# Performance work log

Hardware: AMD Instinct MI355X
Metric: run time of the kernel (lower is better)

The kernel has to match this reference:

```python
import jax, jax.numpy as jnp
import numpy as np

B, S, D, H = 4, 2048, 1024, 16
DQ = D // H  # 64


def setup_inputs() -> dict:
    key = jax.random.key(0)
    ks = jax.random.split(key, 7)
    return {
        "q": jax.random.normal(ks[0], (B, S, D), dtype=jnp.float32),
        "k": jax.random.normal(ks[1], (B, S, D), dtype=jnp.float32),
        "v": jax.random.normal(ks[2], (B, S, D), dtype=jnp.float32),
        "mask": jax.random.randint(ks[3], (B, 1, S, S), 0, 2, dtype=jnp.int32),
        "weight_q": jax.random.normal(ks[4], (H, D, DQ), dtype=jnp.float32),
        "weight_k": jax.random.normal(ks[5], (H, D, DQ), dtype=jnp.float32),
        "weight_v": jax.random.normal(ks[6], (H, D, DQ), dtype=jnp.float32),
    }


def reference(q, k, v, mask, weight_q, weight_k, weight_v):
    # Per-head projections: [b,s,d] x [h,d,q] -> [b,h,s,q]
    Q = jnp.einsum('bsd,hdq->bhsq', q, weight_q)
    K = jnp.einsum('bsd,hdq->bhsq', k, weight_k)
    V = jnp.einsum('bsd,hdq->bhsq', v, weight_v)
    scale = 1.0 / jnp.sqrt(jnp.float32(DQ))
    scores = jnp.einsum('bhsq,bhtq->bhst', Q, K) * scale  # [b,h,s,s]
    scores = jnp.where(mask == 0, jnp.float32(-1e9), scores)
    scores = jax.nn.softmax(scores, axis=-1)
    # Faithful to torch.einsum('bhss,bhsq->bhsq', ...): repeated index 's'
    # takes the DIAGONAL of the attention matrix, scaling V elementwise.
    diag = jnp.diagonal(scores, axis1=2, axis2=3)  # [b,h,s]
    x = diag[..., None] * V  # [b,h,s,dq]
    return x
```

## Files before the change

kernel.cpp:

```cpp
#include <hip/hip_runtime.h>


#define BB 4
#define SS 2048
#define DD 1024
#define HH 16
#define DQQ 64

typedef unsigned short u16;
typedef unsigned int u32;
typedef __attribute__((ext_vector_type(8))) short bf16x8;
typedef __attribute__((ext_vector_type(4))) float f32x4;

static constexpr float SCALE_L2E = 0.125f * 1.44269504f;
static constexpr float NEG9 = -1e9f;

#define MFMA16(a, b, c) __builtin_amdgcn_mfma_f32_16x16x32_bf16((a), (b), (c), 0, 0, 0)

__device__ __forceinline__ float ex2(float x) {
#if __has_builtin(__builtin_amdgcn_exp2f)
    return __builtin_amdgcn_exp2f(x);
#else
    return __expf(x * 0.69314718055994531f);
#endif
}

__device__ __forceinline__ u16 bfrne(float x) {
    u32 u = __float_as_uint(x);
    return (u16)((u + 0x7fffu + ((u >> 16) & 1u)) >> 16);
}
__device__ __forceinline__ u32 pk2(float a, float b) {
    return (u32)bfrne(a) | ((u32)bfrne(b) << 16);
}
__device__ __forceinline__ float lo_f(u32 p) { return __uint_as_float(p << 16); }
__device__ __forceinline__ float hi_f(u32 p) { return __uint_as_float(p & 0xFFFF0000u); }

union U4V { u32 u[4]; bf16x8 v; uint4 q4; };

__global__ __launch_bounds__(256) void mask_pack_k(const int* __restrict__ mask,
                                                   u32* __restrict__ bits) {
    const int w = blockIdx.x * 256 + threadIdx.x;
    const long long row  = (long long)(w >> 6);
    const long long base = row * SS + (long long)((w & 63) << 5);
    const int4* mp = reinterpret_cast<const int4*>(mask + base);
    u32 v = 0;
#pragma unroll
    for (int j = 0; j < 8; ++j) {
        int4 m4 = mp[j];
        v |= (m4.x != 0 ? 1u : 0u) << (4 * j + 0);
        v |= (m4.y != 0 ? 1u : 0u) << (4 * j + 1);
        v |= (m4.z != 0 ? 1u : 0u) << (4 * j + 2);
        v |= (m4.w != 0 ? 1u : 0u) << (4 * j + 3);
    }
    bits[w] = v;
}

__global__ __launch_bounds__(256) void wsplit2_k(const float* __restrict__ W,
                                                 u16* __restrict__ Ph,
                                                 u16* __restrict__ Pl,
                                                 int has_lo, float scale) {
    const int f = blockIdx.x * 4 + (threadIdx.x >> 6);
    const int lane = threadIdx.x & 63;
    const int qtile = f >> 5, kc = f & 31;
    const int h = qtile >> 2, q = ((qtile & 3) << 4) + (lane & 15);
    const int d0 = kc * 32 + (lane >> 4) * 8;
    float x[8];
#pragma unroll
    for (int j = 0; j < 8; ++j)
        x[j] = W[((long long)h * DD + d0 + j) * DQQ + q] * scale;
    U4V hh;
    hh.u[0] = pk2(x[0], x[1]); hh.u[1] = pk2(x[2], x[3]);
    hh.u[2] = pk2(x[4], x[5]); hh.u[3] = pk2(x[6], x[7]);
    const long long base = ((long long)f << 9) + lane * 8;
    *reinterpret_cast<uint4*>(Ph + base) = hh.q4;
    if (has_lo) {
        U4V ll;
        ll.u[0] = pk2(x[0] - lo_f(hh.u[0]), x[1] - hi_f(hh.u[0]));
        ll.u[1] = pk2(x[2] - lo_f(hh.u[1]), x[3] - hi_f(hh.u[1]));
        ll.u[2] = pk2(x[4] - lo_f(hh.u[2]), x[5] - hi_f(hh.u[2]));
        ll.u[3] = pk2(x[6] - lo_f(hh.u[3]), x[7] - hi_f(hh.u[3]));
        *reinterpret_cast<uint4*>(Pl + base) = ll.q4;
    }
}

__global__ __launch_bounds__(256) void splitx_k(const float* __restrict__ X,
                                                u16* __restrict__ Xh,
                                                u16* __restrict__ Xl,
                                                int has_lo) {
    const int g = blockIdx.x * 256 + threadIdx.x;
    const int kc = g & 31;
    const int row = g >> 5;
    const float* xp = X + ((long long)row << 10) + kc * 32;
    const int lrow = row & 15;
    const long long base = (((long long)(row >> 4) * 32 + kc) << 9);
    float4 f[8];
#pragma unroll
    for (int i = 0; i < 8; ++i) f[i] = reinterpret_cast<const float4*>(xp)[i];
#pragma unroll
    for (int lg = 0; lg < 4; ++lg) {
        const float v0 = f[2 * lg].x, v1 = f[2 * lg].y, v2 = f[2 * lg].z, v3 = f[2 * lg].w;
        const float v4 = f[2 * lg + 1].x, v5 = f[2 * lg + 1].y,
                    v6 = f[2 * lg + 1].z, v7 = f[2 * lg + 1].w;
        U4V hh;
        hh.u[0] = pk2(v0, v1); hh.u[1] = pk2(v2, v3);
        hh.u[2] = pk2(v4, v5); hh.u[3] = pk2(v6, v7);
        const long long o = base + (lrow + 16 * lg) * 8;
        *reinterpret_cast<uint4*>(Xh + o) = hh.q4;
        if (has_lo) {
            U4V ll;
            ll.u[0] = pk2(v0 - lo_f(hh.u[0]), v1 - hi_f(hh.u[0]));
            ll.u[1] = pk2(v2 - lo_f(hh.u[1]), v3 - hi_f(hh.u[1]));
            ll.u[2] = pk2(v4 - lo_f(hh.u[2]), v5 - hi_f(hh.u[2]));
            ll.u[3] = pk2(v6 - lo_f(hh.u[3]), v7 - hi_f(hh.u[3]));
            *reinterpret_cast<uint4*>(Xl + o) = ll.q4;
        }
    }
}

__global__ __launch_bounds__(256) void proj_qk2_k(
        const u16* __restrict__ Xh, const u16* __restrict__ Xl,
        const u16* __restrict__ Wph, const u16* __restrict__ Wpl,
        u16* __restrict__ Oh, u16* __restrict__ Ol) {
    const int t = threadIdx.x, lane = t & 63, wid = t >> 6;
    const int lrow = lane & 15, lgrp = lane >> 4;
    const int qt0 = blockIdx.y * 8 + (wid >> 1) * 4;
    const int st0 = blockIdx.x * 8 + (wid & 1) * 4;

    f32x4 acc[4][4];
#pragma unroll
    for (int i = 0; i < 4; ++i)
#pragma unroll
        for (int j = 0; j < 4; ++j) acc[i][j] = (f32x4){0.f, 0.f, 0.f, 0.f};

#pragma unroll 2
    for (int kc = 0; kc < 32; ++kc) {
        bf16x8 Ah[4], Al[4], Bh[4], Bl[4];
#pragma unroll
        for (int mt = 0; mt < 4; ++mt) {
            const long long ab = (((long long)(qt0 + mt) * 32 + kc) << 9) + lane * 8;
            Ah[mt] = *reinterpret_cast<const bf16x8*>(Wph + ab);
            Al[mt] = *reinterpret_cast<const bf16x8*>(Wpl + ab);
        }
#pragma unroll
        for (int nt = 0; nt < 4; ++nt) {
            const long long bb = (((long long)(st0 + nt) * 32 + kc) << 9) + lane * 8;
            Bh[nt] = *reinterpret_cast<const bf16x8*>(Xh + bb);
            Bl[nt] = *reinterpret_cast<const bf16x8*>(Xl + bb);
        }
#pragma unroll
        for (int mt = 0; mt < 4; ++mt)
#pragma unroll
            for (int nt = 0; nt < 4; ++nt) {
                acc[mt][nt] = MFMA16(Ah[mt], Bh[nt], acc[mt][nt]);
                acc[mt][nt] = MFMA16(Ah[mt], Bl[nt], acc[mt][nt]);
                acc[mt][nt] = MFMA16(Al[mt], Bh[nt], acc[mt][nt]);
            }
    }

#pragma unroll
    for (int mt = 0; mt < 4; ++mt) {
        const int qtg = qt0 + mt;
        const int hh_ = qtg >> 2;
        const int qb = ((qtg & 3) << 4) + (lgrp << 2);
#pragma unroll
        for (int nt = 0; nt < 4; ++nt) {
            const int c = (st0 + nt) * 16 + lrow;
            const int b = c >> 11, s = c & 2047;
            const int bh = (b << 4) + hh_;
            const float x0 = acc[mt][nt][0], x1 = acc[mt][nt][1],
                        x2 = acc[mt][nt][2], x3 = acc[mt][nt][3];
            const u32 h01 = pk2(x0, x1), h23 = pk2(x2, x3);
            const u32 l01 = pk2(x0 - lo_f(h01), x1 - hi_f(h01));
            const u32 l23 = pk2(x2 - lo_f(h23), x3 - hi_f(h23));
            const int st = s >> 4, kcq = qb >> 5;
            const int lanep = lrow + (((qb & 31) >> 3) << 4);
            const long long oi = ((((long long)bh * 128 + st) * 2 + kcq) << 9)
                                 + lanep * 8 + (qb & 7);
            *reinterpret_cast<uint2*>(Oh + oi) = make_uint2(h01, h23);
            *reinterpret_cast<uint2*>(Ol + oi) = make_uint2(l01, l23);
        }
    }
}

__global__ __launch_bounds__(256) void proj_v2_k(
        const u16* __restrict__ Xh, const u16* __restrict__ Wph,
        u16* __restrict__ Vb) {
    const int t = threadIdx.x, lane = t & 63, wid = t >> 6;
    const int lrow = lane & 15, lgrp = lane >> 4;
    const int qt0 = blockIdx.y * 8 + (wid >> 1) * 4;
    const int st0 = blockIdx.x * 8 + (wid & 1) * 4;

    f32x4 acc[4][4];
#pragma unroll
    for (int i = 0; i < 4; ++i)
#pragma unroll
        for (int j = 0; j < 4; ++j) acc[i][j] = (f32x4){0.f, 0.f, 0.f, 0.f};

#pragma unroll 2
    for (int kc = 0; kc < 32; ++kc) {
        bf16x8 Ah[4], Bh[4];
#pragma unroll
        for (int mt = 0; mt < 4; ++mt) {
            const long long ab = (((long long)(qt0 + mt) * 32 + kc) << 9) + lane * 8;
            Ah[mt] = *reinterpret_cast<const bf16x8*>(Wph + ab);
        }
#pragma unroll
        for (int nt = 0; nt < 4; ++nt) {
            const long long bb = (((long long)(st0 + nt) * 32 + kc) << 9) + lane * 8;
            Bh[nt] = *reinterpret_cast<const bf16x8*>(Xh + bb);
        }
#pragma unroll
        for (int mt = 0; mt < 4; ++mt)
#pragma unroll
            for (int nt = 0; nt < 4; ++nt)
                acc[mt][nt] = MFMA16(Ah[mt], Bh[nt], acc[mt][nt]);
    }

#pragma unroll
    for (int mt = 0; mt < 4; ++mt) {
        const int qtg = qt0 + mt;
        const int hh_ = qtg >> 2;
        const int qb = ((qtg & 3) << 4) + (lgrp << 2);
#pragma unroll
        for (int nt = 0; nt < 4; ++nt) {
            const int c = (st0 + nt) * 16 + lrow;
            const int b = c >> 11, s = c & 2047;
            const int bh = (b << 4) + hh_;
            const u32 h01 = pk2(acc[mt][nt][0], acc[mt][nt][1]);
            const u32 h23 = pk2(acc[mt][nt][2], acc[mt][nt][3]);
            const long long oi = ((long long)bh * SS + s) * DQQ + qb;
            *reinterpret_cast<uint2*>(Vb + oi) = make_uint2(h01, h23);
        }
    }
}

__global__ __launch_bounds__(256) void attn_k(
        const u16* __restrict__ Qh, const u16* __restrict__ Ql,
        const u16* __restrict__ Kh, const u16* __restrict__ Kl,
        const u16* __restrict__ Vb, const u32* __restrict__ bits,
        float* __restrict__ out) {
    const int qt = blockIdx.x, h = blockIdx.y, b = blockIdx.z;
    const int s0 = qt * 128;
    const long long bh = b * HH + h;
    const int t = threadIdx.x, lane = t & 63, wid = t >> 6;
    const int l15 = lane & 15, lgrp = lane >> 4;

    __shared__ u16 Kst[2][4096];
    __shared__ float sdiag[128];
    __shared__ float dwgt[128];

    bf16x8 qfh[2][2], qfl[2][2];
#pragma unroll
    for (int mt = 0; mt < 2; ++mt)
#pragma unroll
        for (int ks = 0; ks < 2; ++ks) {
            const int stq = qt * 8 + wid * 2 + mt;
            const long long gi = (((bh * 128 + stq) * 2 + ks) << 9) + lane * 8;
            qfh[mt][ks] = *reinterpret_cast<const bf16x8*>(&Qh[gi]);
            qfl[mt][ks] = *reinterpret_cast<const bf16x8*>(&Ql[gi]);
        }

    const u32 kbase = (u32)(bh * 131072u) + (u32)t * 8u;
    const u32 kfb   = (u32)(bh * 131072u) + (u32)lane * 8u;
    bf16x8 sh[2];
    auto loadK = [&](int cchN) {
        const u32 o = kbase + (u32)cchN * 4096u;
        sh[0] = *reinterpret_cast<const bf16x8*>(Kh + o);
        sh[1] = *reinterpret_cast<const bf16x8*>(Kh + o + 2048u);
    };
    auto stageK = [&](int buf) {
        *reinterpret_cast<bf16x8*>(&Kst[buf][t * 8]) = sh[0];
        *reinterpret_cast<bf16x8*>(&Kst[buf][(t + 256) * 8]) = sh[1];
    };

    const u32* __restrict__ brow = bits + (((long long)b * SS + s0) << 6);
    u32 moff[2][4];
#pragma unroll
    for (int mt = 0; mt < 2; ++mt)
#pragma unroll
        for (int r = 0; r < 4; ++r)
            moff[mt][r] = (u32)((wid * 32 + mt * 16 + lgrp * 4 + r) << 6);

    const f32x4 zz = (f32x4){0.f, 0.f, 0.f, 0.f};

    loadK(2 * qt);     stageK(0);
    loadK(2 * qt + 1); stageK(1);
    __syncthreads();
    {
        const int bufA = wid >> 1;
        const int nt0 = (wid & 1) * 2;
        const int cA = 2 * qt + bufA;
#pragma unroll
        for (int mt = 0; mt < 2; ++mt) {
            const int ntd = nt0 + mt;
            const u32 ol = kfb + (u32)cA * 4096u + (u32)(ntd * 2) * 512u;
            bf16x8 kh0 = *reinterpret_cast<const bf16x8*>(&Kst[bufA][(ntd * 2 + 0) * 512 + lane * 8]);
            bf16x8 kh1 = *reinterpret_cast<const bf16x8*>(&Kst[bufA][(ntd * 2 + 1) * 512 + lane * 8]);
            bf16x8 kl0 = *reinterpret_cast<const bf16x8*>(Kl + ol);
            bf16x8 kl1 = *reinterpret_cast<const bf16x8*>(Kl + ol + 512u);
            f32x4 a = MFMA16(qfh[mt][0], kh0, zz);
            a = MFMA16(qfh[mt][1], kh1, a);
            a = MFMA16(qfh[mt][0], kl0, a);
            a = MFMA16(qfh[mt][1], kl1, a);
            a = MFMA16(qfl[mt][0], kh0, a);
            a = MFMA16(qfl[mt][1], kh1, a);
#pragma unroll
            for (int r = 0; r < 4; ++r) {
                if (l15 == lgrp * 4 + r) {
                    const u32 word = brow[moff[mt][r] + (u32)(cA * 2) + (u32)(ntd >> 1)];
                    const u32 bit = (word >> ((ntd & 1) * 16 + l15)) & 1u;
                    sdiag[wid * 32 + mt * 16 + lgrp * 4 + r] = bit ? a[r] : NEG9;
                }
            }
        }
    }
    __syncthreads();

    float sdA[2][4], nsd[2][4];
    f32x4 msd[2];
#pragma unroll
    for (int mt = 0; mt < 2; ++mt) {
        float4 v4 = *reinterpret_cast<const float4*>(&sdiag[wid * 32 + mt * 16 + lgrp * 4]);
        sdA[mt][0] = v4.x; sdA[mt][1] = v4.y; sdA[mt][2] = v4.z; sdA[mt][3] = v4.w;
#pragma unroll
        for (int r = 0; r < 4; ++r) {
            nsd[mt][r] = NEG9 - sdA[mt][r];
            msd[mt][r] = -sdA[mt][r];
        }
    }

    loadK(0); stageK(0);
    float srun[2][4];
#pragma unroll
    for (int mt = 0; mt < 2; ++mt)
#pragma unroll
        for (int r = 0; r < 4; ++r) srun[mt][r] = 0.f;

    for (int cch = 0; cch < 32; ++cch) {
        const int cur = cch & 1;
        __syncthreads();
        if (cch + 1 < 32) loadK(cch + 1);

        bf16x8 kfl[4][2];
        const u32 ko = kfb + (u32)cch * 4096u;
#pragma unroll
        for (int nt = 0; nt < 4; ++nt)
#pragma unroll
            for (int ks = 0; ks < 2; ++ks)
                kfl[nt][ks] = *reinterpret_cast<const bf16x8*>(Kl + ko + (u32)(nt * 2 + ks) * 512u);

        uint2 mw[2][4];
        const u32 c2 = (u32)(cch * 2);
#pragma unroll
        for (int mt = 0; mt < 2; ++mt)
#pragma unroll
            for (int r = 0; r < 4; ++r)
                mw[mt][r] = *reinterpret_cast<const uint2*>(brow + moff[mt][r] + c2);

        bf16x8 kfh[4][2];
#pragma unroll
        for (int nt = 0; nt < 4; ++nt)
#pragma unroll
            for (int ks = 0; ks < 2; ++ks)
                kfh[nt][ks] = *reinterpret_cast<const bf16x8*>(&Kst[cur][(nt * 2 + ks) * 512 + lane * 8]);

        f32x4 sc[2][4];
#pragma unroll
        for (int mt = 0; mt < 2; ++mt)
#pragma unroll
            for (int nt = 0; nt < 4; ++nt) {
                f32x4 a = MFMA16(qfh[mt][0], kfh[nt][0], msd[mt]);
                a = MFMA16(qfh[mt][1], kfh[nt][1], a);
                a = MFMA16(qfh[mt][0], kfl[nt][0], a);
                a = MFMA16(qfh[mt][1], kfl[nt][1], a);
                a = MFMA16(qfl[mt][0], kfh[nt][0], a);
                a = MFMA16(qfl[mt][1], kfh[nt][1], a);
                sc[mt][nt] = a;
            }

#pragma unroll
        for (int mt = 0; mt < 2; ++mt)
#pragma unroll
            for (int r = 0; r < 4; ++r) {
                const u32 w0s = mw[mt][r].x >> l15;
                const u32 w1s = mw[mt][r].y >> l15;
                const float nd = nsd[mt][r];
                float d0 = (w0s & 1u)       ? sc[mt][0][r] : nd;
                float d1 = (w0s & 0x10000u) ? sc[mt][1][r] : nd;
                float d2 = (w1s & 1u)       ? sc[mt][2][r] : nd;
                float d3 = (w1s & 0x10000u) ? sc[mt][3][r] : nd;
                srun[mt][r] += (ex2(d0) + ex2(d1)) + (ex2(d2) + ex2(d3));
            }

        if (cch + 1 < 32) stageK(cur ^ 1);
    }

#pragma unroll
    for (int mt = 0; mt < 2; ++mt)
#pragma unroll
        for (int r = 0; r < 4; ++r) {
            float so = srun[mt][r];
#pragma unroll
            for (int st = 1; st < 16; st <<= 1)
                so += __shfl_xor(so, st, 64);
            if (l15 == 0)
                dwgt[wid * 32 + mt * 16 + lgrp * 4 + r] = 1.0f / so;
        }
    __syncthreads();

    const int orow = t >> 1, oc = (t & 1) * 32;
    const float w = dwgt[orow];
    const u16* vp = Vb + (bh * SS + s0 + orow) * DQQ + oc;
    float* op = out + (bh * SS + s0 + orow) * DQQ + oc;
#pragma unroll
    for (int j = 0; j < 8; ++j) {
        u32 pv = *reinterpret_cast<const u32*>(&vp[j * 4 + 0]);
        u32 pv2 = *reinterpret_cast<const u32*>(&vp[j * 4 + 2]);
        float4 o;
        o.x = lo_f(pv) * w;  o.y = hi_f(pv) * w;
        o.z = lo_f(pv2) * w; o.w = hi_f(pv2) * w;
        reinterpret_cast<float4*>(op)[j] = o;
    }
}

extern "C" void kernel_launch(void* const* d_in, const int* in_sizes, int n_in,
                              void* d_out, int out_size, void* d_ws, size_t ws_size,
                              hipStream_t stream) {
    (void)in_sizes; (void)n_in; (void)out_size; (void)ws_size;
    const float* q    = (const float*)d_in[0];
    const float* k    = (const float*)d_in[1];
    const float* v    = (const float*)d_in[2];
    const int*   mask = (const int*)d_in[3];
    const float* wq   = (const float*)d_in[4];
    const float* wk   = (const float*)d_in[5];
    const float* wv   = (const float*)d_in[6];

    const size_t NP2 = (size_t)BB * HH * SS * DQQ * 2;
    char* wsp = (char*)d_ws;
    u16* Qh = (u16*)wsp;            wsp += NP2;
    u16* Ql = (u16*)wsp;            wsp += NP2;
    u16* Kh = (u16*)wsp;            wsp += NP2;
    u16* Kl = (u16*)wsp;            wsp += NP2;
    u16* Vb = (u16*)wsp;            wsp += NP2;
    u16* Wph = (u16*)wsp;           wsp += (size_t)3 * 2048 * 512 * 2;
    u16* Wpl = (u16*)wsp;           wsp += (size_t)2 * 2048 * 512 * 2;
    u32* bits = (u32*)wsp;          wsp += (size_t)BB * SS * 64 * 4;
    u16* extra = (u16*)wsp;

    u16* Xh_q = Kh;    u16* Xl_q = Kl;
    u16* Xh_k = Vb;    u16* Xl_k = extra;
    u16* Xh_v = extra;

    mask_pack_k<<<dim3(2048), dim3(256), 0, stream>>>(mask, bits);
    wsplit2_k<<<dim3(512), dim3(256), 0, stream>>>(wq, Wph, Wpl, 1, SCALE_L2E);
    wsplit2_k<<<dim3(512), dim3(256), 0, stream>>>(wk, Wph + (1 << 20), Wpl + (1 << 20), 1, 1.0f);
    wsplit2_k<<<dim3(512), dim3(256), 0, stream>>>(wv, Wph + (2u << 20), Wph, 0, 1.0f);

    splitx_k<<<dim3(1024), dim3(256), 0, stream>>>(q, Xh_q, Xl_q, 1);
    proj_qk2_k<<<dim3(64, 8), dim3(256), 0, stream>>>(Xh_q, Xl_q, Wph, Wpl, Qh, Ql);

    splitx_k<<<dim3(1024), dim3(256), 0, stream>>>(k, Xh_k, Xl_k, 1);
    proj_qk2_k<<<dim3(64, 8), dim3(256), 0, stream>>>(Xh_k, Xl_k,
                                                      Wph + (1 << 20), Wpl + (1 << 20),
                                                      Kh, Kl);

    splitx_k<<<dim3(1024), dim3(256), 0, stream>>>(v, Xh_v, Xh_v, 0);
    proj_v2_k<<<dim3(64, 8), dim3(256), 0, stream>>>(Xh_v, Wph + (2u << 20), Vb);

    attn_k<<<dim3(16, 16, 4), dim3(256), 0, stream>>>(Qh, Ql, Kh, Kl, Vb, bits,
                                                      (float*)d_out);
}
```

Before: 337.9 us.

## Halve attention query tile to 64 rows per block and double the grid

The attention kernel now gives each block 64 query rows instead of 128, one 16-row MFMA tile per wave, and launches twice as many blocks. The diagonal score is now computed from K read directly from global memory rather than staged in LDS. The inner loop fuses MFMA and exp accumulation per column tile, which cuts register pressure. The aim is more occupancy and parallelism. The cost is that each K chunk staged in LDS is reused across half as many query rows, doubling K traffic from global memory and L2.

After: 343.5 us. No clear change (+1.6%).

```diff
diff --git a/kernel.cpp b/kernel.cpp
--- a/kernel.cpp
+++ b/kernel.cpp
@@ -240,180 +240,133 @@
         const u16* __restrict__ Vb, const u32* __restrict__ bits,
         float* __restrict__ out) {
     const int qt = blockIdx.x, h = blockIdx.y, b = blockIdx.z;
-    const int s0 = qt * 128;
+    const int s0 = qt * 64;
     const long long bh = b * HH + h;
     const int t = threadIdx.x, lane = t & 63, wid = t >> 6;
     const int l15 = lane & 15, lgrp = lane >> 4;
 
     __shared__ u16 Kst[2][4096];
-    __shared__ float sdiag[128];
-    __shared__ float dwgt[128];
-
-    bf16x8 qfh[2][2], qfl[2][2];
-#pragma unroll
-    for (int mt = 0; mt < 2; ++mt)
-#pragma unroll
-        for (int ks = 0; ks < 2; ++ks) {
-            const int stq = qt * 8 + wid * 2 + mt;
-            const long long gi = (((bh * 128 + stq) * 2 + ks) << 9) + lane * 8;
-            qfh[mt][ks] = *reinterpret_cast<const bf16x8*>(&Qh[gi]);
-            qfl[mt][ks] = *reinterpret_cast<const bf16x8*>(&Ql[gi]);
-        }
+    __shared__ float sdiag[64];
+    __shared__ float dwgt[64];
+
+    bf16x8 qfh[2], qfl[2];
+#pragma unroll
+    for (int ks = 0; ks < 2; ++ks) {
+        const int stq = qt * 4 + wid;
+        const long long gi = (((bh * 128 + stq) * 2 + ks) << 9) + lane * 8;
+        qfh[ks] = *reinterpret_cast<const bf16x8*>(&Qh[gi]);
+        qfl[ks] = *reinterpret_cast<const bf16x8*>(&Ql[gi]);
+    }
 
     const u32 kbase = (u32)(bh * 131072u) + (u32)t * 8u;
     const u32 kfb   = (u32)(bh * 131072u) + (u32)lane * 8u;
-    bf16x8 sh[2];
+    bf16x8 sh0, sh1;
     auto loadK = [&](int cchN) {
         const u32 o = kbase + (u32)cchN * 4096u;
-        sh[0] = *reinterpret_cast<const bf16x8*>(Kh + o);
-        sh[1] = *reinterpret_cast<const bf16x8*>(Kh + o + 2048u);
+        sh0 = *reinterpret_cast<const bf16x8*>(Kh + o);
+        sh1 = *reinterpret_cast<const bf16x8*>(Kh + o + 2048u);
     };
     auto stageK = [&](int buf) {
-        *reinterpret_cast<bf16x8*>(&Kst[buf][t * 8]) = sh[0];
-        *reinterpret_cast<bf16x8*>(&Kst[buf][(t + 256) * 8]) = sh[1];
+        *reinterpret_cast<bf16x8*>(&Kst[buf][t * 8]) = sh0;
+        *reinterpret_cast<bf16x8*>(&Kst[buf][(t + 256) * 8]) = sh1;
     };
 
     const u32* __restrict__ brow = bits + (((long long)b * SS + s0) << 6);
-    u32 moff[2][4];
-#pragma unroll
-    for (int mt = 0; mt < 2; ++mt)
-#pragma unroll
-        for (int r = 0; r < 4; ++r)
-            moff[mt][r] = (u32)((wid * 32 + mt * 16 + lgrp * 4 + r) << 6);
+    u32 moff[4];
+#pragma unroll
+    for (int r = 0; r < 4; ++r)
+        moff[r] = (u32)((wid * 16 + lgrp * 4 + r) << 6);
 
     const f32x4 zz = (f32x4){0.f, 0.f, 0.f, 0.f};
 
-    loadK(2 * qt);     stageK(0);
-    loadK(2 * qt + 1); stageK(1);
+    {
+        const int cA = qt, ntd = wid;
+        const u32 o = kfb + (u32)cA * 4096u + (u32)(ntd * 2) * 512u;
+        bf16x8 kh0 = *reinterpret_cast<const bf16x8*>(Kh + o);
+        bf16x8 kh1 = *reinterpret_cast<const bf16x8*>(Kh + o + 512u);
+        bf16x8 kl0 = *reinterpret_cast<const bf16x8*>(Kl + o);
+        bf16x8 kl1 = *reinterpret_cast<const bf16x8*>(Kl + o + 512u);
+        f32x4 a = MFMA16(qfh[0], kh0, zz);
+        a = MFMA16(qfh[1], kh1, a);
+        a = MFMA16(qfh[0], kl0, a);
+        a = MFMA16(qfh[1], kl1, a);
+        a = MFMA16(qfl[0], kh0, a);
+        a = MFMA16(qfl[1], kh1, a);
+#pragma unroll
+        for (int r = 0; r < 4; ++r) {
+            if (l15 == lgrp * 4 + r) {
+                const u32 word = brow[moff[r] + (u32)(cA * 2) + (u32)(ntd >> 1)];
+                const u32 bit = (word >> ((ntd & 1) * 16 + l15)) & 1u;
+                sdiag[wid * 16 + lgrp * 4 + r] = bit ? a[r] : NEG9;
+            }
+        }
+    }
     __syncthreads();
+
+    float nsd[4];
+    f32x4 msd;
     {
-        const int bufA = wid >> 1;
-        const int nt0 = (wid & 1) * 2;
-        const int cA = 2 * qt + bufA;
-#pragma unroll
-        for (int mt = 0; mt < 2; ++mt) {
-            const int ntd = nt0 + mt;
-            const u32 ol = kfb + (u32)cA * 4096u + (u32)(ntd * 2) * 512u;
-            bf16x8 kh0 = *reinterpret_cast<const bf16x8*>(&Kst[bufA][(ntd * 2 + 0) * 512 + lane * 8]);
-            bf16x8 kh1 = *reinterpret_cast<const bf16x8*>(&Kst[bufA][(ntd * 2 + 1) * 512 + lane * 8]);
-            bf16x8 kl0 = *reinterpret_cast<const bf16x8*>(Kl + ol);
-            bf16x8 kl1 = *reinterpret_cast<const bf16x8*>(Kl + ol + 512u);
-            f32x4 a = MFMA16(qfh[mt][0], kh0, zz);
-            a = MFMA16(qfh[mt][1], kh1, a);
-            a = MFMA16(qfh[mt][0], kl0, a);
-            a = MFMA16(qfh[mt][1], kl1, a);
-            a = MFMA16(qfl[mt][0], kh0, a);
-            a = MFMA16(qfl[mt][1], kh1, a);
-#pragma unroll
-            for (int r = 0; r < 4; ++r) {
-                if (l15 == lgrp * 4 + r) {
-                    const u32 word = brow[moff[mt][r] + (u32)(cA * 2) + (u32)(ntd >> 1)];
-                    const u32 bit = (word >> ((ntd & 1) * 16 + l15)) & 1u;
-                    sdiag[wid * 32 + mt * 16 + lgrp * 4 + r] = bit ? a[r] : NEG9;
-                }
-            }
-        }
-    }
-    __syncthreads();
-
-    float sdA[2][4], nsd[2][4];
-    f32x4 msd[2];
-#pragma unroll
-    for (int mt = 0; mt < 2; ++mt) {
-        float4 v4 = *reinterpret_cast<const float4*>(&sdiag[wid * 32 + mt * 16 + lgrp * 4]);
-        sdA[mt][0] = v4.x; sdA[mt][1] = v4.y; sdA[mt][2] = v4.z; sdA[mt][3] = v4.w;
-#pragma unroll
-        for (int r = 0; r < 4; ++r) {
-            nsd[mt][r] = NEG9 - sdA[mt][r];
-            msd[mt][r] = -sdA[mt][r];
-        }
+        float4 v4 = *reinterpret_cast<const float4*>(&sdiag[wid * 16 + lgrp * 4]);
+        msd[0] = -v4.x; msd[1] = -v4.y; msd[2] = -v4.z; msd[3] = -v4.w;
+        nsd[0] = NEG9 - v4.x; nsd[1] = NEG9 - v4.y;
+        nsd[2] = NEG9 - v4.z; nsd[3] = NEG9 - v4.w;
     }
 
     loadK(0); stageK(0);
-    float srun[2][4];
-#pragma unroll
-    for (int mt = 0; mt < 2; ++mt)
-#pragma unroll
-        for (int r = 0; r < 4; ++r) srun[mt][r] = 0.f;
+    float srun[4] = {0.f, 0.f, 0.f, 0.f};
 
     for (int cch = 0; cch < 32; ++cch) {
         const int cur = cch & 1;
         __syncthreads();
         if (cch + 1 < 32) loadK(cch + 1);
 
-        bf16x8 kfl[4][2];
+        uint2 mw[4];
+        const u32 c2 = (u32)(cch * 2);
+#pragma unroll
+        for (int r = 0; r < 4; ++r)
+            mw[r] = *reinterpret_cast<const uint2*>(brow + moff[r] + c2);
+
         const u32 ko = kfb + (u32)cch * 4096u;
 #pragma unroll
-        for (int nt = 0; nt < 4; ++nt)
-#pragma unroll
-            for (int ks = 0; ks < 2; ++ks)
-                kfl[nt][ks] = *reinterpret_cast<const bf16x8*>(Kl + ko + (u32)(nt * 2 + ks) * 512u);
-
-        uint2 mw[2][4];
-        const u32 c2 = (u32)(cch * 2);
-#pragma unroll
-        for (int mt = 0; mt < 2; ++mt)
-#pragma unroll
-            for (int r = 0; r < 4; ++r)
-                mw[mt][r] = *reinterpret_cast<const uint2*>(brow + moff[mt][r] + c2);
-
-        bf16x8 kfh[4][2];
-#pragma unroll
-        for (int nt = 0; nt < 4; ++nt)
-#pragma unroll
-            for (int ks = 0; ks < 2; ++ks)
-                kfh[nt][ks] = *reinterpret_cast<const bf16x8*>(&Kst[cur][(nt * 2 + ks) * 512 + lane * 8]);
-
-        f32x4 sc[2][4];
-#pragma unroll
-        for (int mt = 0; mt < 2; ++mt)
-#pragma unroll
-            for (int nt = 0; nt < 4; ++nt) {
-                f32x4 a = MFMA16(qfh[mt][0], kfh[nt][0], msd[mt]);
-                a = MFMA16(qfh[mt][1], kfh[nt][1], a);
-                a = MFMA16(qfh[mt][0], kfl[nt][0], a);
-                a = MFMA16(qfh[mt][1], kfl[nt][1], a);
-                a = MFMA16(qfl[mt][0], kfh[nt][0], a);
-                a = MFMA16(qfl[mt][1], kfh[nt][1], a);
-                sc[mt][nt] = a;
+        for (int nt = 0; nt < 4; ++nt) {
+            bf16x8 kh0 = *reinterpret_cast<const bf16x8*>(&Kst[cur][(nt * 2 + 0) * 512 + lane * 8]);
+            bf16x8 kh1 = *reinterpret_cast<const bf16x8*>(&Kst[cur][(nt * 2 + 1) * 512 + lane * 8]);
+            bf16x8 kl0 = *reinterpret_cast<const bf16x8*>(Kl + ko + (u32)(nt * 2 + 0) * 512u);
+            bf16x8 kl1 = *reinterpret_cast<const bf16x8*>(Kl + ko + (u32)(nt * 2 + 1) * 512u);
+            f32x4 a = MFMA16(qfh[0], kh0, msd);
+            a = MFMA16(qfh[1], kh1, a);
+            a = MFMA16(qfh[0], kl0, a);
+            a = MFMA16(qfh[1], kl1, a);
+            a = MFMA16(qfl[0], kh0, a);
+            a = MFMA16(qfl[1], kh1, a);
+#pragma unroll
+            for (int r = 0; r < 4; ++r) {
+                const u32 w = (nt < 2) ? mw[r].x : mw[r].y;
+                const float d = ((w >> ((nt & 1) * 16 + l15)) & 1u) ? a[r] : nsd[r];
+                srun[r] += ex2(d);
             }
-
-#pragma unroll
-        for (int mt = 0; mt < 2; ++mt)
-#pragma unroll
-            for (int r = 0; r < 4; ++r) {
-                const u32 w0s = mw[mt][r].x >> l15;
-                const u32 w1s = mw[mt][r].y >> l15;
-                const float nd = nsd[mt][r];
-                float d0 = (w0s & 1u)       ? sc[mt][0][r] : nd;
-                float d1 = (w0s & 0x10000u) ? sc[mt][1][r] : nd;
-                float d2 = (w1s & 1u)       ? sc[mt][2][r] : nd;
-                float d3 = (w1s & 0x10000u) ? sc[mt][3][r] : nd;
-                srun[mt][r] += (ex2(d0) + ex2(d1)) + (ex2(d2) + ex2(d3));
-            }
+        }
 
         if (cch + 1 < 32) stageK(cur ^ 1);
     }
 
 #pragma unroll
-    for (int mt = 0; mt < 2; ++mt)
-#pragma unroll
-        for (int r = 0; r < 4; ++r) {
-            float so = srun[mt][r];
-#pragma unroll
-            for (int st = 1; st < 16; st <<= 1)
-                so += __shfl_xor(so, st, 64);
-            if (l15 == 0)
-                dwgt[wid * 32 + mt * 16 + lgrp * 4 + r] = 1.0f / so;
-        }
+    for (int r = 0; r < 4; ++r) {
+        float so = srun[r];
+#pragma unroll
+        for (int st = 1; st < 16; st <<= 1)
+            so += __shfl_xor(so, st, 64);
+        if (l15 == 0)
+            dwgt[wid * 16 + lgrp * 4 + r] = 1.0f / so;
+    }
     __syncthreads();
 
-    const int orow = t >> 1, oc = (t & 1) * 32;
+    const int orow = t >> 2, oc = (t & 3) * 16;
     const float w = dwgt[orow];
     const u16* vp = Vb + (bh * SS + s0 + orow) * DQQ + oc;
     float* op = out + (bh * SS + s0 + orow) * DQQ + oc;
 #pragma unroll
-    for (int j = 0; j < 8; ++j) {
+    for (int j = 0; j < 4; ++j) {
         u32 pv = *reinterpret_cast<const u32*>(&vp[j * 4 + 0]);
         u32 pv2 = *reinterpret_cast<const u32*>(&vp[j * 4 + 2]);
         float4 o;
@@ -467,6 +420,6 @@
     splitx_k<<<dim3(1024), dim3(256), 0, stream>>>(v, Xh_v, Xh_v, 0);
     proj_v2_k<<<dim3(64, 8), dim3(256), 0, stream>>>(Xh_v, Wph + (2u << 20), Vb);
 
-    attn_k<<<dim3(16, 16, 4), dim3(256), 0, stream>>>(Qh, Ql, Kh, Kl, Vb, bits,
+    attn_k<<<dim3(32, 16, 4), dim3(256), 0, stream>>>(Qh, Ql, Kh, Kl, Vb, bits,
                                                       (float*)d_out);
 }
```
